# Performance work log

Hardware: AMD Instinct MI355X
Metric: run time of the kernel (lower is better)

## Reference

```python
import jax, jax.numpy as jnp
from jax import lax
import numpy as np

N_ATOMS, N_BONDS, N_GRAPHS = 8192, 32768, 256
EMBED, HIDDEN, DEPTH = 32, 256, 10
ATOM_VOCAB, BOND_VOCAB = 200, 10


def setup_inputs() -> dict:
    key = jax.random.key(0)
    ks = jax.random.split(key, 16)
    f = lambda k, *sh: jax.random.normal(k, sh, dtype=jnp.float32) * 0.05
    return {
        "atom_features": jax.random.randint(ks[0], (N_ATOMS,), 0, ATOM_VOCAB),
        "bond_features": jax.random.randint(ks[1], (N_BONDS,), 0, BOND_VOCAB),
        "adjacency_matrix": jax.random.randint(ks[2], (N_ATOMS, N_ATOMS), 0, 2, dtype=jnp.int32),
        "batch_indices": jax.random.randint(ks[3], (N_ATOMS,), 0, N_GRAPHS),
        "atom_emb": f(ks[4], ATOM_VOCAB, EMBED),
        "bond_emb": f(ks[5], BOND_VOCAB, EMBED),
        "msg_W": f(ks[6], DEPTH, HIDDEN, 2 * EMBED),
        "msg_b": f(ks[7], DEPTH, HIDDEN),
        "gru_Wih": f(ks[8], DEPTH, 3 * EMBED, HIDDEN),
        "gru_Whh": f(ks[9], DEPTH, 3 * EMBED, EMBED),
        "gru_bih": f(ks[10], DEPTH, 3 * EMBED),
        "gru_bhh": f(ks[11], DEPTH, 3 * EMBED),
        "pool_W": f(ks[12], HIDDEN, EMBED),
        "pool_b": f(ks[13], HIDDEN),
    }


def _gmpn(atom_emb, bond_emb, msg_W, msg_b, gru_Wih, gru_Whh, gru_bih, gru_bhh,
          pool_W, pool_b, atom_features, bond_features, adjacency_matrix, batch_indices):
    H = atom_emb[atom_features]                       # [N, E]
    A = (adjacency_matrix > 0).astype(H.dtype)        # [N, N] 0/1
    deg = A.sum(axis=1)                               # [N]
    has_nb = deg > 0
    inv_deg = jnp.where(has_nb, 1.0 / jnp.maximum(deg, 1.0), 0.0)[:, None]

    def layer(h, params):
        W, b, wih, whh, b_ih, b_hh = params
        # mean_j Linear([h_i ; h_j]) = W1 h_i + W2 mean_j h_j + b
        neigh_mean = (A @ h) * inv_deg                # [N, E]
        W1, W2 = W[:, :EMBED], W[:, EMBED:]
        msg = h @ W1.T + neigh_mean @ W2.T + b        # [N, HIDDEN]
        msg = jnp.where(has_nb[:, None], msg, 0.0)    # zero message if no neighbors
        # single-step GRU: input=msg, hidden state=h
        gi = msg @ wih.T + b_ih
        gh = h @ whh.T + b_hh
        ir, iz, inn = jnp.split(gi, 3, axis=-1)
        hr, hz, hn = jnp.split(gh, 3, axis=-1)
        r = jax.nn.sigmoid(ir + hr)
        z = jax.nn.sigmoid(iz + hz)
        n = jnp.tanh(inn + r * hn)
        h_new = (1.0 - z) * n + z * h                 # [N, E]
        return h_new, None

    H, _ = lax.scan(layer, H, (msg_W, msg_b, gru_Wih, gru_Whh, gru_bih, gru_bhh))

    # per-graph mean pooling (zeros for empty graphs), then global_pool linear
    seg_sum = jax.ops.segment_sum(H, batch_indices, num_segments=N_GRAPHS)
    cnt = jax.ops.segment_sum(jnp.ones((H.shape[0],), H.dtype), batch_indices, num_segments=N_GRAPHS)
    graph_mean = jnp.where(cnt[:, None] > 0, seg_sum / jnp.maximum(cnt, 1.0)[:, None], 0.0)
    graph_embeddings = graph_mean @ pool_W.T + pool_b  # [G, HIDDEN]

    bond_embeddings = bond_emb[bond_features]          # [B, E]
    return H, bond_embeddings, graph_embeddings


def reference(atom_features, bond_features, adjacency_matrix, batch_indices,
              atom_emb, bond_emb, msg_W, msg_b, gru_Wih, gru_Whh, gru_bih, gru_bhh,
              pool_W, pool_b):
    return _gmpn(atom_emb, bond_emb, msg_W, msg_b, gru_Wih, gru_Whh, gru_bih, gru_bhh,
                 pool_W, pool_b, atom_features, bond_features, adjacency_matrix, batch_indices)
```

## Files before the change

### kernel.cpp

```cpp
#include <hip/hip_runtime.h>
#include <stdint.h>

typedef __bf16 bf16x8 __attribute__((ext_vector_type(8)));
typedef float f32x4 __attribute__((ext_vector_type(4)));

__device__ __forceinline__ float b2f(unsigned short u){
  unsigned int t = ((unsigned int)u) << 16;
  return __builtin_bit_cast(float, t);
}
__device__ __forceinline__ unsigned short f2b(float f){
  unsigned int x = __builtin_bit_cast(unsigned int, f);
  x = x + 0x7FFFu + ((x >> 16) & 1u);
  return (unsigned short)(x >> 16);
}
__device__ __forceinline__ void spread8(unsigned int B, unsigned int w[4]){
  unsigned int m = __umul24(B, 0x8001u);
  w[0] = __umul24(m & 0x00010001u, 0x3F80u);
  w[1] = __umul24(m & 0x00040004u, 0x0FE0u);
  w[2] = __umul24(m & 0x00100010u, 0x03F8u);
  w[3] = __umul24(m & 0x00400040u, 0x00FEu);
}
__device__ __forceinline__ float fsig(float x){ return 1.f/(1.f + __expf(-x)); }
__device__ __forceinline__ float ftanh(float x){ return 1.f - 2.f/(__expf(2.f*x) + 1.f); }

__device__ __forceinline__ void gload_lds16(const void* gsrc, void* ldst){
  __builtin_amdgcn_global_load_lds(
      (const __attribute__((address_space(1))) unsigned int*)gsrc,
      (__attribute__((address_space(3))) unsigned int*)ldst,
      16, 0, 0);
}

__device__ __forceinline__ const char* stage_src(int s,
    const char* mW, const char* wi, const char* wh,
    const char* mb, const char* bi, const char* bh){
  if (s >= 5664) s = 5600;
  int o = s*16;
  if (o < 32768){ int a = o ^ ((((unsigned)o>>7)&7)<<4); return mW + a; }
  if (o < 81920){ int a = o - 32768; a ^= (((unsigned)a>>9)&7)<<4; return wi + a; }
  if (o < 89600){ int a = o - 81920; int row = a/80; int col = a - row*80;
                  if (col >= 64) col = 0; return wh + row*64 + col; }
  int a = o - 89600;
  if (a < 512)  return mb + a;
  if (a < 704)  return bi + (a - 512);
  if (a < 896)  return bh + (a - 704);
  return mb;
}

__global__ void k_prep(const void* s_msgW, const void* s_msgb, const void* s_wih,
                       const void* s_whh, const void* s_bih, const void* s_bhh,
                       const void* s_poolW, const void* s_poolb,
                       const unsigned short* __restrict__ aemb_u16,
                       unsigned short* __restrict__ cw,
                       int* __restrict__ deg, float* __restrict__ seg,
                       float* __restrict__ cnt, int* __restrict__ flag){
  int b = blockIdx.x, t = threadIdx.x;
  unsigned int uu = aemb_u16[2*t];
  int e = (int)((uu >> 7) & 0xFF);
  unsigned long long vote = __ballot(e >= 100 && e <= 127);
  int isb = (__popcll(vote) > 32) ? 1 : 0;
  if (b < 1771){
    int id = b*256 + t;
    if (id < 453248){
      const void* src; int off;
      if      (id < 163840){ src = s_msgW;  off = id; }
      else if (id < 166400){ src = s_msgb;  off = id - 163840; }
      else if (id < 412160){ src = s_wih;   off = id - 166400; }
      else if (id < 442880){ src = s_whh;   off = id - 412160; }
      else if (id < 443840){ src = s_bih;   off = id - 442880; }
      else if (id < 444800){ src = s_bhh;   off = id - 443840; }
      else if (id < 452992){ src = s_poolW; off = id - 444800; }
      else                 { src = s_poolb; off = id - 452992; }
      cw[id] = isb ? ((const unsigned short*)src)[off]
                   : f2b(((const float*)src)[off]);
    }
  } else {
    int id2 = (b - 1771)*256 + t;
    if (id2 < 8192){ deg[id2] = 0; seg[id2] = 0.f; }
    if (id2 < 256) cnt[id2] = 0.f;
    if (b == 1771 && t == 0) flag[0] = isb;
  }
}

__global__ void k_pack(const int* __restrict__ adj, unsigned int* __restrict__ mask3,
                       int* __restrict__ deg){
  int tid = blockIdx.x*256 + threadIdx.x;
  int rb  = tid >> 12;
  int rem = tid & 4095;
  int kgg = rem >> 6;
  int L   = rem & 63;
  int lc = L & 15, q = L >> 4;
  int row = rb*16 + lc;
  const int4* p4 = (const int4*)(adj + (size_t)row*8192 + kgg*128 + q*8);
  unsigned int dw = 0; int pc = 0;
  #pragma unroll
  for (int s=0;s<4;s++){
    int4 u = p4[s*8];
    int4 v = p4[s*8 + 1];
    unsigned int b = (unsigned int)(u.x > 0)
                   | ((unsigned int)(u.y > 0) << 1)
                   | ((unsigned int)(u.z > 0) << 2)
                   | ((unsigned int)(u.w > 0) << 3)
                   | ((unsigned int)(v.x > 0) << 4)
                   | ((unsigned int)(v.y > 0) << 5)
                   | ((unsigned int)(v.z > 0) << 6)
                   | ((unsigned int)(v.w > 0) << 7);
    dw |= b << (8*s);
    pc += __popc(b);
  }
  mask3[tid] = dw;
  pc += __shfl_xor(pc, 16);
  pc += __shfl_xor(pc, 32);
  if (q == 0) atomicAdd(deg + row, pc);
}

__global__ void k_bond(const int* __restrict__ bft, const void* __restrict__ braw,
                       const int* __restrict__ flag,
                       unsigned short* __restrict__ outB16, float* __restrict__ outB32){
  int id = blockIdx.x*256 + threadIdx.x;
  int e = id >> 5, c = id & 31;
  int idx = bft[e]*32 + c;
  if (flag[0]) outB16[id] = ((const unsigned short*)braw)[idx];
  else         outB32[id] = ((const float*)braw)[idx];
}

__global__ void k_embed(const int* __restrict__ af, const void* __restrict__ araw,
                        const int* __restrict__ flag,
                        float* __restrict__ hf32, uint4* __restrict__ hfrag){
  __shared__ __align__(16) float sh[512];
  int t = threadIdx.x;
  int r = t >> 5, c = t & 31;
  int row = blockIdx.x*16 + r;
  int idx = af[row]*32 + c;
  float f;
  if (flag[0]) f = b2f(((const unsigned short*)araw)[idx]);
  else         f = ((const float*)araw)[idx];
  hf32[row*32 + c] = f;
  sh[r*32 + c] = f;
  __syncthreads();
  if (t < 64){
    int nt = t >> 5, Lq = t & 31;
    int ks32 = blockIdx.x >> 1, half = blockIdx.x & 1;
    int col = nt*16 + (Lq & 15);
    int rbase = (Lq >> 4)*8;
    unsigned int w[4];
    #pragma unroll
    for (int p=0;p<4;p++){
      unsigned int lo = f2b(sh[(rbase + 2*p    )*32 + col]);
      unsigned int hi = f2b(sh[(rbase + 2*p + 1)*32 + col]);
      w[p] = lo | (hi << 16);
    }
    hfrag[(ks32*2 + nt)*64 + half*32 + Lq] = make_uint4(w[0],w[1],w[2],w[3]);
  }
}

#define NEIGH_STEP(MW0, MW1, P0, P1)                                        \
  _Pragma("unroll")                                                         \
  for (int s=0; s<4; s++){                                                  \
    union { unsigned int u[4]; bf16x8 v; } A0, A1, B0, B1;                  \
    spread8((MW0 >> (8*s)) & 0xFFu, A0.u);                                  \
    spread8((MW1 >> (8*s)) & 0xFFu, A1.u);                                  \
    B0.u[0]=P0[s].x; B0.u[1]=P0[s].y; B0.u[2]=P0[s].z; B0.u[3]=P0[s].w;     \
    B1.u[0]=P1[s].x; B1.u[1]=P1[s].y; B1.u[2]=P1[s].z; B1.u[3]=P1[s].w;     \
    a00 = __builtin_amdgcn_mfma_f32_16x16x32_bf16(A0.v, B0.v, a00, 0,0,0);  \
    a01 = __builtin_amdgcn_mfma_f32_16x16x32_bf16(A0.v, B1.v, a01, 0,0,0);  \
    a10 = __builtin_amdgcn_mfma_f32_16x16x32_bf16(A1.v, B0.v, a10, 0,0,0);  \
    a11 = __builtin_amdgcn_mfma_f32_16x16x32_bf16(A1.v, B1.v, a11, 0,0,0);  \
  }

__launch_bounds__(512, 2)
__global__ void k_layer(const unsigned int* __restrict__ mask3,
                        const uint4* __restrict__ hfragIn,
                        unsigned int* __restrict__ hfragOut,
                        float* __restrict__ hf32,
                        const int* __restrict__ deg,
                        const unsigned short* __restrict__ msgW,
                        const unsigned short* __restrict__ msgb,
                        const unsigned short* __restrict__ wih,
                        const unsigned short* __restrict__ whh,
                        const unsigned short* __restrict__ bih,
                        const unsigned short* __restrict__ bhh,
                        const int* __restrict__ bidx,
                        float* __restrict__ seg, float* __restrict__ cnt,
                        unsigned short* __restrict__ out16, float* __restrict__ out32,
                        const int* __restrict__ flag, int last)
{
  __shared__ __align__(16) char uni[33792];
  __shared__ __align__(16) unsigned short sA[32][72];
  __shared__ __align__(16) unsigned short smsg[32][264];
  __shared__ __align__(16) char wlds[91136];
  __shared__ int sdeg[32];

  const int t = threadIdx.x;
  const int b = blockIdx.x;
  const int w = t >> 6, L = t & 63;
  const int q = L >> 4, lc = L & 15;
  const int rowbase = b*32;

  const int r0 = t >> 4;
  const int cl = t & 15;
  const int r  = rowbase + r0;
  const int isb = flag[0];
  const int dgr = deg[r];
  const float invr = dgr > 0 ? 1.f/(float)dgr : 0.f;
  float h0 = hf32[r*32 + cl];
  float h1 = hf32[r*32 + 16 + cl];
  sA[r0][cl]    = f2b(h0);
  sA[r0][16+cl] = f2b(h1);
  if (cl == 0) sdeg[r0] = dgr;

  {
    f32x4 a00={0,0,0,0}, a01={0,0,0,0}, a10={0,0,0,0}, a11={0,0,0,0};
    const unsigned int* mp = mask3 + (size_t)b*8192 + w*512 + L;
    const uint4* bp = hfragIn + (size_t)w*4096 + L;

    uint4 pa0[4], pa1[4], pb0[4], pb1[4];
    unsigned int ma0, ma1, mb0, mb1;
    ma0 = mp[0];  ma1 = mp[4096];
    mb0 = mp[64]; mb1 = mp[4096 + 64];
    #pragma unroll
    for (int s=0;s<4;s++){ pa0[s]=bp[s*128];     pa1[s]=bp[s*128 + 64]; }
    #pragma unroll
    for (int s=0;s<4;s++){ pb0[s]=bp[(4+s)*128]; pb1[s]=bp[(4+s)*128 + 64]; }

    {
      const char* mW = (const char*)msgW;
      const char* wi = (const char*)wih;
      const char* wh = (const char*)whh;
      const char* mb = (const char*)msgb;
      const char* bi = (const char*)bih;
      const char* bh = (const char*)bhh;
      #pragma unroll
      for (int it=0; it<12; ++it){
        int base = it*512 + w*64;
        if (base < 5696){
          int s = base + L;
          const char* src = stage_src(s, mW, wi, wh, mb, bi, bh);
          gload_lds16(src, wlds + (size_t)base*16 + (size_t)L*16);
        }
      }
    }

    #pragma unroll
    for (int g=0; g<8; g+=2){
      NEIGH_STEP(ma0, ma1, pa0, pa1);
      if (g+2 < 8){
        ma0 = mp[(g+2)*64]; ma1 = mp[4096 + (g+2)*64];
        #pragma unroll
        for (int s=0;s<4;s++){ int ks=(g+2)*4+s; pa0[s]=bp[ks*128]; pa1[s]=bp[ks*128+64]; }
      }
      NEIGH_STEP(mb0, mb1, pb0, pb1);
      if (g+3 < 8){
        mb0 = mp[(g+3)*64]; mb1 = mp[4096 + (g+3)*64];
        #pragma unroll
        for (int s=0;s<4;s++){ int ks=(g+3)*4+s; pb0[s]=bp[ks*128]; pb1[s]=bp[ks*128+64]; }
      }
    }

    float* sp = (float*)uni + w*1056;
    #pragma unroll
    for (int rg=0; rg<4; rg++){
      int rw = q*4 + rg;
      sp[rw*33 + lc]         = a00[rg];
      sp[rw*33 + 16 + lc]    = a01[rg];
      sp[(16+rw)*33 + lc]    = a10[rg];
      sp[(16+rw)*33 + 16+lc] = a11[rg];
    }
  }
  __syncthreads();
  {
    const float* spf = (const float*)uni;
    float s0 = 0.f, s1 = 0.f;
    #pragma unroll
    for (int ww=0; ww<8; ww++){
      s0 += spf[ww*1056 + r0*33 + cl];
      s1 += spf[ww*1056 + r0*33 + 16 + cl];
    }
    sA[r0][32+cl] = f2b(s0*invr);
    sA[r0][48+cl] = f2b(s1*invr);
  }
  __syncthreads();
  {
    int rt = w & 1, ntb = (w >> 1)*4;
    int sw = (lc & 7) << 4;
    union { uint4 u; bf16x8 v; } A0, A1;
    A0.u = *(const uint4*)&sA[rt*16 + lc][q*8];
    A1.u = *(const uint4*)&sA[rt*16 + lc][32 + q*8];
    #pragma unroll
    for (int i=0; i<4; i++){
      int nt = ntb + i;
      int abase = (nt*16 + lc)*128 + q*16;
      union { uint4 u; bf16x8 v; } B0, B1;
      B0.u = *(const uint4*)(wlds + ((abase     ) ^ sw));
      B1.u = *(const uint4*)(wlds + ((abase + 64) ^ sw));
      f32x4 am = {0,0,0,0};
      am = __builtin_amdgcn_mfma_f32_16x16x32_bf16(A0.v, B0.v, am, 0,0,0);
      am = __builtin_amdgcn_mfma_f32_16x16x32_bf16(A1.v, B1.v, am, 0,0,0);
      float bv = b2f(*(const unsigned short*)(wlds + 89600 + (nt*16 + lc)*2));
      #pragma unroll
      for (int rg=0; rg<4; rg++){
        int rw = rt*16 + q*4 + rg;
        float v = am[rg] + bv;
        if (sdeg[rw] == 0) v = 0.f;
        smsg[rw][nt*16 + lc] = f2b(v);
      }
    }
  }
  __syncthreads();
  {
    float* sgi = (float*)uni;
    float* sgh = (float*)(uni + 12800);
    if (w < 6){
      int nt = w;
      int sw = (lc & 7) << 4;
      f32x4 g0 = {0,0,0,0}, g1 = {0,0,0,0};
      #pragma unroll
      for (int ks=0; ks<8; ks++){
        union { uint4 u; bf16x8 v; } A0, A1, B;
        int al = (nt*16 + lc)*512 + ks*64 + q*16;
        B.u  = *(const uint4*)(wlds + 32768 + (al ^ sw));
        A0.u = *(const uint4*)&smsg[lc][ks*32 + q*8];
        A1.u = *(const uint4*)&smsg[16 + lc][ks*32 + q*8];
        g0 = __builtin_amdgcn_mfma_f32_16x16x32_bf16(A0.v, B.v, g0, 0,0,0);
        g1 = __builtin_amdgcn_mfma_f32_16x16x32_bf16(A1.v, B.v, g1, 0,0,0);
      }
      #pragma unroll
      for (int rg=0; rg<4; rg++){
        sgi[(q*4+rg)*100      + nt*16 + lc] = g0[rg];
        sgi[(16+q*4+rg)*100   + nt*16 + lc] = g1[rg];
      }
    } else {
      int rt = w - 6;
      union { uint4 u; bf16x8 v; } A;
      A.u = *(const uint4*)&sA[rt*16 + lc][q*8];
      #pragma unroll
      for (int nt=0; nt<6; nt++){
        union { uint4 u; bf16x8 v; } B;
        B.u = *(const uint4*)(wlds + 81920 + (nt*16 + lc)*80 + q*16);
        f32x4 hh = {0,0,0,0};
        hh = __builtin_amdgcn_mfma_f32_16x16x32_bf16(A.v, B.v, hh, 0,0,0);
        #pragma unroll
        for (int rg=0; rg<4; rg++)
          sgh[(rt*16 + q*4+rg)*100 + nt*16 + lc] = hh[rg];
      }
    }
  }
  __syncthreads();
  {
    const float* sgi = (const float*)uni;
    const float* sgh = (const float*)(uni + 12800);
    const unsigned short* bihL = (const unsigned short*)(wlds + 90112);
    const unsigned short* bhhL = (const unsigned short*)(wlds + 90304);
    float ir0 = sgi[r0*100 + cl]    + b2f(bihL[cl]),    hr0 = sgh[r0*100 + cl]    + b2f(bhhL[cl]);
    float iz0 = sgi[r0*100 + 32+cl] + b2f(bihL[32+cl]), hz0 = sgh[r0*100 + 32+cl] + b2f(bhhL[32+cl]);
    float in0 = sgi[r0*100 + 64+cl] + b2f(bihL[64+cl]), hn0 = sgh[r0*100 + 64+cl] + b2f(bhhL[64+cl]);
    float ir1 = sgi[r0*100 + 16+cl] + b2f(bihL[16+cl]), hr1 = sgh[r0*100 + 16+cl] + b2f(bhhL[16+cl]);
    float iz1 = sgi[r0*100 + 48+cl] + b2f(bihL[48+cl]), hz1 = sgh[r0*100 + 48+cl] + b2f(bhhL[48+cl]);
    float in1 = sgi[r0*100 + 80+cl] + b2f(bihL[80+cl]), hn1 = sgh[r0*100 + 80+cl] + b2f(bhhL[80+cl]);
    float rr0 = fsig(ir0 + hr0), zz0 = fsig(iz0 + hz0);
    float rr1 = fsig(ir1 + hr1), zz1 = fsig(iz1 + hz1);
    float nn0 = ftanh(in0 + rr0*hn0);
    float nn1 = ftanh(in1 + rr1*hn1);
    h0 = (1.f - zz0)*nn0 + zz0*h0;
    h1 = (1.f - zz1)*nn1 + zz1*h1;
    hf32[r*32 + cl]      = h0;
    hf32[r*32 + 16 + cl] = h1;
    unsigned int m0 = f2b(h0), m1 = f2b(h1);
    unsigned int p0 = (unsigned int)__shfl_xor((int)m0, 16);
    unsigned int p1 = (unsigned int)__shfl_xor((int)m1, 16);
    if ((r & 1) == 0){
      int ks32 = r >> 5;
      int Lf = ((r >> 3) & 3)*16 + cl;
      int pidx = (r & 7) >> 1;
      hfragOut[((ks32*2 + 0)*64 + Lf)*4 + pidx] = m0 | (p0 << 16);
      hfragOut[((ks32*2 + 1)*64 + Lf)*4 + pidx] = m1 | (p1 << 16);
    }
    if (last){
      if (isb){ out16[r*32 + cl] = (unsigned short)m0; out16[r*32 + 16 + cl] = (unsigned short)m1; }
      else    { out32[r*32 + cl] = h0; out32[r*32 + 16 + cl] = h1; }
      int gb = bidx[r];
      atomicAdd(seg + gb*32 + cl, h0);
      atomicAdd(seg + gb*32 + 16 + cl, h1);
      if (cl == 0) atomicAdd(cnt + gb, 1.f);
    }
  }
}

__global__ void k_pool(const float* __restrict__ seg, const float* __restrict__ cnt,
                       const unsigned short* __restrict__ pw, const unsigned short* __restrict__ pb,
                       const int* __restrict__ flag,
                       unsigned short* __restrict__ outG16, float* __restrict__ outG32){
  int g = blockIdx.x, o = threadIdx.x;
  float cv = cnt[g];
  float ic = cv > 0.f ? 1.f/cv : 0.f;
  float s = 0.f;
  #pragma unroll
  for (int c=0;c<32;c++) s += seg[g*32+c]*ic*b2f(pw[o*32+c]);
  s += b2f(pb[o]);
  if (flag[0]) outG16[g*256 + o] = f2b(s);
  else         outG32[g*256 + o] = s;
}

extern "C" void kernel_launch(void* const* d_in, const int* in_sizes, int n_in,
                              void* d_out, int out_size, void* d_ws, size_t ws_size,
                              hipStream_t stream){
  const int* af   = (const int*)d_in[0];
  const int* bft  = (const int*)d_in[1];
  const int* adj  = (const int*)d_in[2];
  const int* bidx = (const int*)d_in[3];

  char* ws = (char*)d_ws;
  unsigned int*   mask3  = (unsigned int*)(ws + 0);
  unsigned int*   hfrag0 = (unsigned int*)(ws + 8388608);
  unsigned int*   hfrag1 = (unsigned int*)(ws + 8912896);
  float*          hf32   = (float*)(ws + 9437184);
  int*            deg    = (int*)(ws + 10485760);
  float*          seg    = (float*)(ws + 10518528);
  float*          cnt    = (float*)(ws + 10551296);
  int*            flag   = (int*)(ws + 10552320);
  unsigned short* cw     = (unsigned short*)(ws + 10552384);

  unsigned short* o16 = (unsigned short*)d_out;
  float*          o32 = (float*)d_out;

  k_prep<<<1803, 256, 0, stream>>>(d_in[6], d_in[7], d_in[8], d_in[9], d_in[10],
                                   d_in[11], d_in[12], d_in[13],
                                   (const unsigned short*)d_in[4],
                                   cw, deg, seg, cnt, flag);
  k_pack<<<8192, 256, 0, stream>>>(adj, mask3, deg);
  k_bond<<<4096, 256, 0, stream>>>(bft, d_in[5], flag, o16 + 262144, o32 + 262144);
  k_embed<<<512, 512, 0, stream>>>(af, d_in[4], flag, hf32, (uint4*)hfrag0);

  for (int d = 0; d < 10; d++){
    const uint4*  hin  = (const uint4*)((d & 1) ? hfrag1 : hfrag0);
    unsigned int* hout = (d & 1) ? hfrag0 : hfrag1;
    k_layer<<<256, 512, 0, stream>>>(mask3, hin, hout, hf32, deg,
                                     cw + (size_t)d*16384,        cw + 163840 + d*256,
                                     cw + 166400 + (size_t)d*24576, cw + 412160 + d*3072,
                                     cw + 442880 + d*96,          cw + 443840 + d*96,
                                     bidx, seg, cnt, o16, o32, flag, (d == 9) ? 1 : 0);
  }
  k_pool<<<256, 256, 0, stream>>>(seg, cnt, cw + 444800, cw + 452992, flag,
                                  o16 + 1310720, o32 + 1310720);
}
```

Baseline: 536.1 us.

## Fuse ten layer launches into one persistent kernel with grid barrier

The ten per-layer kernel launches are replaced by a single persistent kernel that loops over depth and synchronises all 256 blocks with an atomic grid barrier between layers. Each block keeps its rows' hidden state h in registers across layers, so hf32 is only read once and no longer written back. This removes launch gaps, per-launch prologue work and the fp32 state round trip. In exchange it depends on all 256 blocks being co-resident, which the 2-blocks-per-CU launch bound should allow, and it adds barrier spin latency.

New measurement: 1.055 ms. 1.97x slower.

```diff
diff --git a/kernel.cpp b/kernel.cpp
--- a/kernel.cpp
+++ b/kernel.cpp
@@ -28,6 +28,25 @@
       (const __attribute__((address_space(1))) unsigned int*)gsrc,
       (__attribute__((address_space(3))) unsigned int*)ldst,
       16, 0, 0);
+}
+
+__device__ __forceinline__ void gbar(int* bar, int nb){
+  __syncthreads();
+  if (threadIdx.x == 0){
+    int g = __hip_atomic_load(&bar[1], __ATOMIC_RELAXED, __HIP_MEMORY_SCOPE_AGENT);
+    __threadfence();
+    int a = __hip_atomic_fetch_add(&bar[0], 1, __ATOMIC_ACQ_REL, __HIP_MEMORY_SCOPE_AGENT);
+    if (a == nb - 1){
+      __hip_atomic_store(&bar[0], 0, __ATOMIC_RELAXED, __HIP_MEMORY_SCOPE_AGENT);
+      __hip_atomic_fetch_add(&bar[1], 1, __ATOMIC_RELEASE, __HIP_MEMORY_SCOPE_AGENT);
+    } else {
+      while (__hip_atomic_load(&bar[1], __ATOMIC_ACQUIRE, __HIP_MEMORY_SCOPE_AGENT) == g){
+        __builtin_amdgcn_s_sleep(2);
+      }
+    }
+    __threadfence();
+  }
+  __syncthreads();
 }
 
 __device__ __forceinline__ const char* stage_src(int s,
@@ -77,7 +96,7 @@
     int id2 = (b - 1771)*256 + t;
     if (id2 < 8192){ deg[id2] = 0; seg[id2] = 0.f; }
     if (id2 < 256) cnt[id2] = 0.f;
-    if (b == 1771 && t == 0) flag[0] = isb;
+    if (b == 1771 && t == 0){ flag[0] = isb; flag[4] = 0; flag[5] = 0; }
   }
 }
 
@@ -168,21 +187,16 @@
   }
 
 __launch_bounds__(512, 2)
-__global__ void k_layer(const unsigned int* __restrict__ mask3,
-                        const uint4* __restrict__ hfragIn,
-                        unsigned int* __restrict__ hfragOut,
-                        float* __restrict__ hf32,
-                        const int* __restrict__ deg,
-                        const unsigned short* __restrict__ msgW,
-                        const unsigned short* __restrict__ msgb,
-                        const unsigned short* __restrict__ wih,
-                        const unsigned short* __restrict__ whh,
-                        const unsigned short* __restrict__ bih,
-                        const unsigned short* __restrict__ bhh,
-                        const int* __restrict__ bidx,
-                        float* __restrict__ seg, float* __restrict__ cnt,
-                        unsigned short* __restrict__ out16, float* __restrict__ out32,
-                        const int* __restrict__ flag, int last)
+__global__ void k_layers(const unsigned int* __restrict__ mask3,
+                         unsigned int* __restrict__ hfrag0,
+                         unsigned int* __restrict__ hfrag1,
+                         const float* __restrict__ hf32,
+                         const int* __restrict__ deg,
+                         const unsigned short* __restrict__ cw,
+                         const int* __restrict__ bidx,
+                         float* __restrict__ seg, float* __restrict__ cnt,
+                         unsigned short* __restrict__ out16, float* __restrict__ out32,
+                         const int* __restrict__ flag, int* bar)
 {
   __shared__ __align__(16) char uni[33792];
   __shared__ __align__(16) unsigned short sA[32][72];
@@ -204,31 +218,36 @@
   const float invr = dgr > 0 ? 1.f/(float)dgr : 0.f;
   float h0 = hf32[r*32 + cl];
   float h1 = hf32[r*32 + 16 + cl];
-  sA[r0][cl]    = f2b(h0);
-  sA[r0][16+cl] = f2b(h1);
   if (cl == 0) sdeg[r0] = dgr;
 
-  {
-    f32x4 a00={0,0,0,0}, a01={0,0,0,0}, a10={0,0,0,0}, a11={0,0,0,0};
-    const unsigned int* mp = mask3 + (size_t)b*8192 + w*512 + L;
-    const uint4* bp = hfragIn + (size_t)w*4096 + L;
-
-    uint4 pa0[4], pa1[4], pb0[4], pb1[4];
-    unsigned int ma0, ma1, mb0, mb1;
-    ma0 = mp[0];  ma1 = mp[4096];
-    mb0 = mp[64]; mb1 = mp[4096 + 64];
-    #pragma unroll
-    for (int s=0;s<4;s++){ pa0[s]=bp[s*128];     pa1[s]=bp[s*128 + 64]; }
-    #pragma unroll
-    for (int s=0;s<4;s++){ pb0[s]=bp[(4+s)*128]; pb1[s]=bp[(4+s)*128 + 64]; }
+  for (int d = 0; d < 10; ++d){
+    const char* mW = (const char*)(cw + (size_t)d*16384);
+    const char* mb = (const char*)(cw + 163840 + d*256);
+    const char* wi = (const char*)(cw + 166400 + (size_t)d*24576);
+    const char* wh = (const char*)(cw + 412160 + d*3072);
+    const char* bi = (const char*)(cw + 442880 + d*96);
+    const char* bh = (const char*)(cw + 443840 + d*96);
+    const uint4*  hfragIn  = (const uint4*)((d & 1) ? hfrag1 : hfrag0);
+    unsigned int* hfragOut = (d & 1) ? hfrag0 : hfrag1;
+    const int last = (d == 9);
+
+    sA[r0][cl]    = f2b(h0);
+    sA[r0][16+cl] = f2b(h1);
 
     {
-      const char* mW = (const char*)msgW;
-      const char* wi = (const char*)wih;
-      const char* wh = (const char*)whh;
-      const char* mb = (const char*)msgb;
-      const char* bi = (const char*)bih;
-      const char* bh = (const char*)bhh;
+      f32x4 a00={0,0,0,0}, a01={0,0,0,0}, a10={0,0,0,0}, a11={0,0,0,0};
+      const unsigned int* mp = mask3 + (size_t)b*8192 + w*512 + L;
+      const uint4* bp = hfragIn + (size_t)w*4096 + L;
+
+      uint4 pa0[4], pa1[4], pb0[4], pb1[4];
+      unsigned int ma0, ma1, mb0, mb1;
+      ma0 = mp[0];  ma1 = mp[4096];
+      mb0 = mp[64]; mb1 = mp[4096 + 64];
+      #pragma unroll
+      for (int s=0;s<4;s++){ pa0[s]=bp[s*128];     pa1[s]=bp[s*128 + 64]; }
+      #pragma unroll
+      for (int s=0;s<4;s++){ pb0[s]=bp[(4+s)*128]; pb1[s]=bp[(4+s)*128 + 64]; }
+
       #pragma unroll
       for (int it=0; it<12; ++it){
         int base = it*512 + w*64;
@@ -238,150 +257,150 @@
           gload_lds16(src, wlds + (size_t)base*16 + (size_t)L*16);
         }
       }
-    }
-
-    #pragma unroll
-    for (int g=0; g<8; g+=2){
-      NEIGH_STEP(ma0, ma1, pa0, pa1);
-      if (g+2 < 8){
-        ma0 = mp[(g+2)*64]; ma1 = mp[4096 + (g+2)*64];
+
+      #pragma unroll
+      for (int g=0; g<8; g+=2){
+        NEIGH_STEP(ma0, ma1, pa0, pa1);
+        if (g+2 < 8){
+          ma0 = mp[(g+2)*64]; ma1 = mp[4096 + (g+2)*64];
+          #pragma unroll
+          for (int s=0;s<4;s++){ int ks=(g+2)*4+s; pa0[s]=bp[ks*128]; pa1[s]=bp[ks*128+64]; }
+        }
+        NEIGH_STEP(mb0, mb1, pb0, pb1);
+        if (g+3 < 8){
+          mb0 = mp[(g+3)*64]; mb1 = mp[4096 + (g+3)*64];
+          #pragma unroll
+          for (int s=0;s<4;s++){ int ks=(g+3)*4+s; pb0[s]=bp[ks*128]; pb1[s]=bp[ks*128+64]; }
+        }
+      }
+
+      float* sp = (float*)uni + w*1056;
+      #pragma unroll
+      for (int rg=0; rg<4; rg++){
+        int rw = q*4 + rg;
+        sp[rw*33 + lc]         = a00[rg];
+        sp[rw*33 + 16 + lc]    = a01[rg];
+        sp[(16+rw)*33 + lc]    = a10[rg];
+        sp[(16+rw)*33 + 16+lc] = a11[rg];
+      }
+    }
+    __syncthreads();
+    {
+      const float* spf = (const float*)uni;
+      float s0 = 0.f, s1 = 0.f;
+      #pragma unroll
+      for (int ww=0; ww<8; ww++){
+        s0 += spf[ww*1056 + r0*33 + cl];
+        s1 += spf[ww*1056 + r0*33 + 16 + cl];
+      }
+      sA[r0][32+cl] = f2b(s0*invr);
+      sA[r0][48+cl] = f2b(s1*invr);
+    }
+    __syncthreads();
+    {
+      int rt = w & 1, ntb = (w >> 1)*4;
+      int sw = (lc & 7) << 4;
+      union { uint4 u; bf16x8 v; } A0, A1;
+      A0.u = *(const uint4*)&sA[rt*16 + lc][q*8];
+      A1.u = *(const uint4*)&sA[rt*16 + lc][32 + q*8];
+      #pragma unroll
+      for (int i=0; i<4; i++){
+        int nt = ntb + i;
+        int abase = (nt*16 + lc)*128 + q*16;
+        union { uint4 u; bf16x8 v; } B0, B1;
+        B0.u = *(const uint4*)(wlds + ((abase     ) ^ sw));
+        B1.u = *(const uint4*)(wlds + ((abase + 64) ^ sw));
+        f32x4 am = {0,0,0,0};
+        am = __builtin_amdgcn_mfma_f32_16x16x32_bf16(A0.v, B0.v, am, 0,0,0);
+        am = __builtin_amdgcn_mfma_f32_16x16x32_bf16(A1.v, B1.v, am, 0,0,0);
+        float bv = b2f(*(const unsigned short*)(wlds + 89600 + (nt*16 + lc)*2));
         #pragma unroll
-        for (int s=0;s<4;s++){ int ks=(g+2)*4+s; pa0[s]=bp[ks*128]; pa1[s]=bp[ks*128+64]; }
-      }
-      NEIGH_STEP(mb0, mb1, pb0, pb1);
-      if (g+3 < 8){
-        mb0 = mp[(g+3)*64]; mb1 = mp[4096 + (g+3)*64];
+        for (int rg=0; rg<4; rg++){
+          int rw = rt*16 + q*4 + rg;
+          float v = am[rg] + bv;
+          if (sdeg[rw] == 0) v = 0.f;
+          smsg[rw][nt*16 + lc] = f2b(v);
+        }
+      }
+    }
+    __syncthreads();
+    {
+      float* sgi = (float*)uni;
+      float* sgh = (float*)(uni + 12800);
+      if (w < 6){
+        int nt = w;
+        int sw = (lc & 7) << 4;
+        f32x4 g0 = {0,0,0,0}, g1 = {0,0,0,0};
         #pragma unroll
-        for (int s=0;s<4;s++){ int ks=(g+3)*4+s; pb0[s]=bp[ks*128]; pb1[s]=bp[ks*128+64]; }
-      }
-    }
-
-    float* sp = (float*)uni + w*1056;
-    #pragma unroll
-    for (int rg=0; rg<4; rg++){
-      int rw = q*4 + rg;
-      sp[rw*33 + lc]         = a00[rg];
-      sp[rw*33 + 16 + lc]    = a01[rg];
-      sp[(16+rw)*33 + lc]    = a10[rg];
-      sp[(16+rw)*33 + 16+lc] = a11[rg];
-    }
-  }
-  __syncthreads();
-  {
-    const float* spf = (const float*)uni;
-    float s0 = 0.f, s1 = 0.f;
-    #pragma unroll
-    for (int ww=0; ww<8; ww++){
-      s0 += spf[ww*1056 + r0*33 + cl];
-      s1 += spf[ww*1056 + r0*33 + 16 + cl];
-    }
-    sA[r0][32+cl] = f2b(s0*invr);
-    sA[r0][48+cl] = f2b(s1*invr);
-  }
-  __syncthreads();
-  {
-    int rt = w & 1, ntb = (w >> 1)*4;
-    int sw = (lc & 7) << 4;
-    union { uint4 u; bf16x8 v; } A0, A1;
-    A0.u = *(const uint4*)&sA[rt*16 + lc][q*8];
-    A1.u = *(const uint4*)&sA[rt*16 + lc][32 + q*8];
-    #pragma unroll
-    for (int i=0; i<4; i++){
-      int nt = ntb + i;
-      int abase = (nt*16 + lc)*128 + q*16;
-      union { uint4 u; bf16x8 v; } B0, B1;
-      B0.u = *(const uint4*)(wlds + ((abase     ) ^ sw));
-      B1.u = *(const uint4*)(wlds + ((abase + 64) ^ sw));
-      f32x4 am = {0,0,0,0};
-      am = __builtin_amdgcn_mfma_f32_16x16x32_bf16(A0.v, B0.v, am, 0,0,0);
-      am = __builtin_amdgcn_mfma_f32_16x16x32_bf16(A1.v, B1.v, am, 0,0,0);
-      float bv = b2f(*(const unsigned short*)(wlds + 89600 + (nt*16 + lc)*2));
-      #pragma unroll
-      for (int rg=0; rg<4; rg++){
-        int rw = rt*16 + q*4 + rg;
-        float v = am[rg] + bv;
-        if (sdeg[rw] == 0) v = 0.f;
-        smsg[rw][nt*16 + lc] = f2b(v);
-      }
-    }
-  }
-  __syncthreads();
-  {
-    float* sgi = (float*)uni;
-    float* sgh = (float*)(uni + 12800);
-    if (w < 6){
-      int nt = w;
-      int sw = (lc & 7) << 4;
-      f32x4 g0 = {0,0,0,0}, g1 = {0,0,0,0};
-      #pragma unroll
-      for (int ks=0; ks<8; ks++){
-        union { uint4 u; bf16x8 v; } A0, A1, B;
-        int al = (nt*16 + lc)*512 + ks*64 + q*16;
-        B.u  = *(const uint4*)(wlds + 32768 + (al ^ sw));
-        A0.u = *(const uint4*)&smsg[lc][ks*32 + q*8];
-        A1.u = *(const uint4*)&smsg[16 + lc][ks*32 + q*8];
-        g0 = __builtin_amdgcn_mfma_f32_16x16x32_bf16(A0.v, B.v, g0, 0,0,0);
-        g1 = __builtin_amdgcn_mfma_f32_16x16x32_bf16(A1.v, B.v, g1, 0,0,0);
-      }
-      #pragma unroll
-      for (int rg=0; rg<4; rg++){
-        sgi[(q*4+rg)*100      + nt*16 + lc] = g0[rg];
-        sgi[(16+q*4+rg)*100   + nt*16 + lc] = g1[rg];
-      }
-    } else {
-      int rt = w - 6;
-      union { uint4 u; bf16x8 v; } A;
-      A.u = *(const uint4*)&sA[rt*16 + lc][q*8];
-      #pragma unroll
-      for (int nt=0; nt<6; nt++){
-        union { uint4 u; bf16x8 v; } B;
-        B.u = *(const uint4*)(wlds + 81920 + (nt*16 + lc)*80 + q*16);
-        f32x4 hh = {0,0,0,0};
-        hh = __builtin_amdgcn_mfma_f32_16x16x32_bf16(A.v, B.v, hh, 0,0,0);
+        for (int ks=0; ks<8; ks++){
+          union { uint4 u; bf16x8 v; } A0, A1, B;
+          int al = (nt*16 + lc)*512 + ks*64 + q*16;
+          B.u  = *(const uint4*)(wlds + 32768 + (al ^ sw));
+          A0.u = *(const uint4*)&smsg[lc][ks*32 + q*8];
+          A1.u = *(const uint4*)&smsg[16 + lc][ks*32 + q*8];
+          g0 = __builtin_amdgcn_mfma_f32_16x16x32_bf16(A0.v, B.v, g0, 0,0,0);
+          g1 = __builtin_amdgcn_mfma_f32_16x16x32_bf16(A1.v, B.v, g1, 0,0,0);
+        }
         #pragma unroll
-        for (int rg=0; rg<4; rg++)
-          sgh[(rt*16 + q*4+rg)*100 + nt*16 + lc] = hh[rg];
-      }
-    }
-  }
-  __syncthreads();
-  {
-    const float* sgi = (const float*)uni;
-    const float* sgh = (const float*)(uni + 12800);
-    const unsigned short* bihL = (const unsigned short*)(wlds + 90112);
-    const unsigned short* bhhL = (const unsigned short*)(wlds + 90304);
-    float ir0 = sgi[r0*100 + cl]    + b2f(bihL[cl]),    hr0 = sgh[r0*100 + cl]    + b2f(bhhL[cl]);
-    float iz0 = sgi[r0*100 + 32+cl] + b2f(bihL[32+cl]), hz0 = sgh[r0*100 + 32+cl] + b2f(bhhL[32+cl]);
-    float in0 = sgi[r0*100 + 64+cl] + b2f(bihL[64+cl]), hn0 = sgh[r0*100 + 64+cl] + b2f(bhhL[64+cl]);
-    float ir1 = sgi[r0*100 + 16+cl] + b2f(bihL[16+cl]), hr1 = sgh[r0*100 + 16+cl] + b2f(bhhL[16+cl]);
-    float iz1 = sgi[r0*100 + 48+cl] + b2f(bihL[48+cl]), hz1 = sgh[r0*100 + 48+cl] + b2f(bhhL[48+cl]);
-    float in1 = sgi[r0*100 + 80+cl] + b2f(bihL[80+cl]), hn1 = sgh[r0*100 + 80+cl] + b2f(bhhL[80+cl]);
-    float rr0 = fsig(ir0 + hr0), zz0 = fsig(iz0 + hz0);
-    float rr1 = fsig(ir1 + hr1), zz1 = fsig(iz1 + hz1);
-    float nn0 = ftanh(in0 + rr0*hn0);
-    float nn1 = ftanh(in1 + rr1*hn1);
-    h0 = (1.f - zz0)*nn0 + zz0*h0;
-    h1 = (1.f - zz1)*nn1 + zz1*h1;
-    hf32[r*32 + cl]      = h0;
-    hf32[r*32 + 16 + cl] = h1;
-    unsigned int m0 = f2b(h0), m1 = f2b(h1);
-    unsigned int p0 = (unsigned int)__shfl_xor((int)m0, 16);
-    unsigned int p1 = (unsigned int)__shfl_xor((int)m1, 16);
-    if ((r & 1) == 0){
-      int ks32 = r >> 5;
-      int Lf = ((r >> 3) & 3)*16 + cl;
-      int pidx = (r & 7) >> 1;
-      hfragOut[((ks32*2 + 0)*64 + Lf)*4 + pidx] = m0 | (p0 << 16);
-      hfragOut[((ks32*2 + 1)*64 + Lf)*4 + pidx] = m1 | (p1 << 16);
-    }
-    if (last){
-      if (isb){ out16[r*32 + cl] = (unsigned short)m0; out16[r*32 + 16 + cl] = (unsigned short)m1; }
-      else    { out32[r*32 + cl] = h0; out32[r*32 + 16 + cl] = h1; }
-      int gb = bidx[r];
-      atomicAdd(seg + gb*32 + cl, h0);
-      atomicAdd(seg + gb*32 + 16 + cl, h1);
-      if (cl == 0) atomicAdd(cnt + gb, 1.f);
-    }
+        for (int rg=0; rg<4; rg++){
+          sgi[(q*4+rg)*100      + nt*16 + lc] = g0[rg];
+          sgi[(16+q*4+rg)*100   + nt*16 + lc] = g1[rg];
+        }
+      } else {
+        int rt = w - 6;
+        union { uint4 u; bf16x8 v; } A;
+        A.u = *(const uint4*)&sA[rt*16 + lc][q*8];
+        #pragma unroll
+        for (int nt=0; nt<6; nt++){
+          union { uint4 u; bf16x8 v; } B;
+          B.u = *(const uint4*)(wlds + 81920 + (nt*16 + lc)*80 + q*16);
+          f32x4 hh = {0,0,0,0};
+          hh = __builtin_amdgcn_mfma_f32_16x16x32_bf16(A.v, B.v, hh, 0,0,0);
+          #pragma unroll
+          for (int rg=0; rg<4; rg++)
+            sgh[(rt*16 + q*4+rg)*100 + nt*16 + lc] = hh[rg];
+        }
+      }
+    }
+    __syncthreads();
+    {
+      const float* sgi = (const float*)uni;
+      const float* sgh = (const float*)(uni + 12800);
+      const unsigned short* bihL = (const unsigned short*)(wlds + 90112);
+      const unsigned short* bhhL = (const unsigned short*)(wlds + 90304);
+      float ir0 = sgi[r0*100 + cl]    + b2f(bihL[cl]),    hr0 = sgh[r0*100 + cl]    + b2f(bhhL[cl]);
+      float iz0 = sgi[r0*100 + 32+cl] + b2f(bihL[32+cl]), hz0 = sgh[r0*100 + 32+cl] + b2f(bhhL[32+cl]);
+      float in0 = sgi[r0*100 + 64+cl] + b2f(bihL[64+cl]), hn0 = sgh[r0*100 + 64+cl] + b2f(bhhL[64+cl]);
+      float ir1 = sgi[r0*100 + 16+cl] + b2f(bihL[16+cl]), hr1 = sgh[r0*100 + 16+cl] + b2f(bhhL[16+cl]);
+      float iz1 = sgi[r0*100 + 48+cl] + b2f(bihL[48+cl]), hz1 = sgh[r0*100 + 48+cl] + b2f(bhhL[48+cl]);
+      float in1 = sgi[r0*100 + 80+cl] + b2f(bihL[80+cl]), hn1 = sgh[r0*100 + 80+cl] + b2f(bhhL[80+cl]);
+      float rr0 = fsig(ir0 + hr0), zz0 = fsig(iz0 + hz0);
+      float rr1 = fsig(ir1 + hr1), zz1 = fsig(iz1 + hz1);
+      float nn0 = ftanh(in0 + rr0*hn0);
+      float nn1 = ftanh(in1 + rr1*hn1);
+      h0 = (1.f - zz0)*nn0 + zz0*h0;
+      h1 = (1.f - zz1)*nn1 + zz1*h1;
+      unsigned int m0 = f2b(h0), m1 = f2b(h1);
+      if (!last){
+        unsigned int p0 = (unsigned int)__shfl_xor((int)m0, 16);
+        unsigned int p1 = (unsigned int)__shfl_xor((int)m1, 16);
+        if ((r & 1) == 0){
+          int ks32 = r >> 5;
+          int Lf = ((r >> 3) & 3)*16 + cl;
+          int pidx = (r & 7) >> 1;
+          hfragOut[((ks32*2 + 0)*64 + Lf)*4 + pidx] = m0 | (p0 << 16);
+          hfragOut[((ks32*2 + 1)*64 + Lf)*4 + pidx] = m1 | (p1 << 16);
+        }
+      } else {
+        if (isb){ out16[r*32 + cl] = (unsigned short)m0; out16[r*32 + 16 + cl] = (unsigned short)m1; }
+        else    { out32[r*32 + cl] = h0; out32[r*32 + 16 + cl] = h1; }
+        int gb = bidx[r];
+        atomicAdd(seg + gb*32 + cl, h0);
+        atomicAdd(seg + gb*32 + 16 + cl, h1);
+        if (cl == 0) atomicAdd(cnt + gb, 1.f);
+      }
+    }
+    if (!last) gbar(bar, 256);
   }
 }
 
@@ -421,6 +440,7 @@
 
   unsigned short* o16 = (unsigned short*)d_out;
   float*          o32 = (float*)d_out;
+  int*            bar = flag + 4;
 
   k_prep<<<1803, 256, 0, stream>>>(d_in[6], d_in[7], d_in[8], d_in[9], d_in[10],
                                    d_in[11], d_in[12], d_in[13],
@@ -430,15 +450,9 @@
   k_bond<<<4096, 256, 0, stream>>>(bft, d_in[5], flag, o16 + 262144, o32 + 262144);
   k_embed<<<512, 512, 0, stream>>>(af, d_in[4], flag, hf32, (uint4*)hfrag0);
 
-  for (int d = 0; d < 10; d++){
-    const uint4*  hin  = (const uint4*)((d & 1) ? hfrag1 : hfrag0);
-    unsigned int* hout = (d & 1) ? hfrag0 : hfrag1;
-    k_layer<<<256, 512, 0, stream>>>(mask3, hin, hout, hf32, deg,
-                                     cw + (size_t)d*16384,        cw + 163840 + d*256,
-                                     cw + 166400 + (size_t)d*24576, cw + 412160 + d*3072,
-                                     cw + 442880 + d*96,          cw + 443840 + d*96,
-                                     bidx, seg, cnt, o16, o32, flag, (d == 9) ? 1 : 0);
-  }
+  k_layers<<<256, 512, 0, stream>>>(mask3, hfrag0, hfrag1, hf32, deg, cw,
+                                    bidx, seg, cnt, o16, o32, flag, bar);
+
   k_pool<<<256, 256, 0, stream>>>(seg, cnt, cw + 444800, cw + 452992, flag,
                                   o16 + 1310720, o32 + 1310720);
 }
```
